# Optimization experiments

Hardware: AMD Instinct MI355X
Metric: run time of the kernel (lower is better)

The kernel has to match this reference:

```python
import jax, jax.numpy as jnp
from jax import lax
import numpy as np

NSTEP, NGRID, MU = 365, 4000, 8
STAIND = NSTEP - 1          # time index providing static parameters
TDLST = [1, 2, 3, 4, 5]     # 1-based indices of dynamic parameters
HBV_LO = jnp.array([0.0, 1.0, 0.005, 0.005, 0.0, 0.0, 0.005, 0.005, 0.0, 0.0, 0.0], jnp.float32)
HBV_HI = jnp.array([1.0, 2000.0, 0.995, 0.995, 1.0, 7.0, 0.995, 0.995, 1.0, 1.0, 1.0], jnp.float32)
SMIN = 1e-4                 # clamp floor for states
CAPMIN = 0.005 / 4          # floor for derived capacities

# ---- MARRMoT-style flux helpers (all elementwise) ----

def split_1(p1, In):
    return p1 * In

def soilmoisture_1(S1, S1max, S2, S2max):
    mask = (S1 / S1max < S2 / S2max).astype(S1.dtype)
    return (S2 * S1max - S1 * S2max) / (S1max + S2max) * mask

def soilmoisture_2(S1, S1max, S2, S2max, S3, S3max):
    # water rebalance to equal relative storage (3 stores); flux drawn from S2
    mask = (S1 / S1max < (S2 + S3) / (S2max + S3max)).astype(S1.dtype)
    return (S2 * S1max - S1 * S2max) / (S1max + S2max + S3max) * mask

def evap_7(S, Smax, Ep, dt):
    return jnp.minimum(S / Smax * Ep, S / dt)

def evap_1(S, Ep, dt):
    return jnp.minimum(Ep, S / dt)

def saturation_1(In, S, Smax):
    return In * (S >= Smax).astype(In.dtype)

def interflow_5(p1, S):
    return p1 * S

def baseflow_1(p1, S):
    return p1 * S

def percolation_4(pbase, zperc, rexp, deficit, defmax, S, Smax, dt):
    pc = pbase * (1.0 + zperc * (deficit / defmax) ** (1.0 + rexp)) * S / Smax
    return jnp.maximum(0.0, jnp.minimum(pc, S / dt))

def deficit_dist(S1, S1max, S2, S2max):
    d1 = jnp.maximum(0.0, 1.0 - S1 / S1max)
    d2 = jnp.maximum(0.0, 1.0 - S2 / S2max)
    tot = d1 + d2
    return jnp.where(tot > 0, d1 / jnp.where(tot > 0, tot, 1.0), S1max / (S1max + S2max))


def _forward(x, parameters):
    Nstep, Ngrid = x.shape[0], x.shape[1]
    mu = parameters.shape[3]
    P_ = x[:, :, 0]   # [Nstep, Ngrid]
    Ep_ = x[:, :, 2]  # [Nstep, Ngrid]

    # scale raw [0,1] params to physical ranges
    parT = HBV_LO[None, None, :, None] + parameters * (HBV_HI - HBV_LO)[None, None, :, None]
    parsta = parT[STAIND]  # [Ngrid, 11, mu] static params
    dyn = np.zeros(11, dtype=bool)
    for ix in TDLST:
        dyn[ix - 1] = True
    dyn = jnp.asarray(dyn)
    # dydrop=0 -> dynamic params always used on tdlst slots, static elsewhere
    parhbv = jnp.where(dyn[None, None, :, None], parT, parsta[None])  # [Nstep,Ngrid,11,mu]

    S0 = jnp.full((Ngrid, mu), 0.001, x.dtype)

    def step(carry, inp):
        S1, S2, S3, S4, S5 = carry
        Pt, Ept, par = inp            # par: [Ngrid, 11, mu]
        P = Pt[:, None]               # [Ngrid, 1] broadcasts against [Ngrid, mu]
        Ep = Ept[:, None]
        pctim, smax, f1, f2, kuz, rexp, f3, f4, pfree, klzp, klzs = [par[:, i, :] for i in range(11)]

        uztwm = f1 * smax
        uzfwm = jnp.maximum(CAPMIN, f2 * (smax - uztwm))
        lztwm = jnp.maximum(CAPMIN, f3 * (smax - uztwm - uzfwm))
        lzfwpm = jnp.maximum(CAPMIN, f4 * (smax - uztwm - uzfwm - lztwm))
        lzfwsm = jnp.maximum(CAPMIN, (1.0 - f4) * (smax - uztwm - uzfwm - lztwm))
        pbase = lzfwpm * klzp + lzfwsm * klzs
        denom = lzfwsm * klzs + lzfwpm * klzp
        zperc = jnp.minimum(1e5, (lztwm + lzfwsm * (1.0 - klzs)) / denom + lzfwpm * (1.0 - klzp) / denom)
        dt = 1.0

        flux_qdir = split_1(pctim, P)
        flux_peff = split_1(1.0 - pctim, P)
        flux_ru = soilmoisture_1(S1, uztwm, S2, uzfwm)
        flux_euztw = evap_7(S1, uztwm, Ep, dt)
        flux_twexu = saturation_1(flux_peff, S1, uztwm)
        flux_qsur = saturation_1(flux_twexu, S2, uzfwm)
        flux_qint = interflow_5(kuz, S2)
        flux_euzfw = evap_1(S2, jnp.maximum(0.0, Ep - flux_euztw), dt)
        deficit = (jnp.maximum(1e-8, lztwm - S3) + jnp.maximum(1e-8, lzfwpm - S4)
                   + jnp.maximum(1e-8, lzfwsm - S5))
        defmax = jnp.maximum(1e-8, lztwm + lzfwpm + lzfwsm)
        flux_pc = percolation_4(pbase, zperc, rexp, deficit, defmax, S2, uzfwm, dt)
        flux_pctw = split_1(1.0 - pfree, flux_pc)
        flux_elztw = evap_7(S3, lztwm, jnp.maximum(0.0, Ep - flux_euztw - flux_euzfw), dt)
        flux_twexl = saturation_1(flux_pctw, S3, lztwm)
        fp = deficit_dist(S4, lzfwpm, S5, lzfwsm)
        fs = deficit_dist(S5, lzfwsm, S4, lzfwpm)
        flux_twexlp = split_1(fp, flux_twexl)
        flux_twexls = split_1(fs, flux_twexl)
        flux_pcfwp = split_1(pfree * fp, flux_pc)
        flux_pcfws = split_1(pfree * fs, flux_pc)
        flux_rlp = soilmoisture_2(S3, lztwm, S4, lzfwpm, S5, lzfwsm)
        flux_rls = soilmoisture_2(S3, lztwm, S5, lzfwsm, S4, lzfwpm)
        flux_qbfp = baseflow_1(klzp, S4)
        flux_qbfs = baseflow_1(klzs, S5)

        nS1 = jnp.maximum(S1 + flux_peff + flux_ru - flux_euztw - flux_twexu, SMIN)
        nS2 = jnp.maximum(S2 + flux_twexu - flux_euzfw - flux_qsur - flux_qint - flux_ru - flux_pc, SMIN)
        nS3 = jnp.maximum(S3 + flux_pctw + flux_rlp + flux_rls - flux_elztw - flux_twexl, SMIN)
        nS4 = jnp.maximum(S4 + flux_twexlp + flux_pcfwp - flux_rlp - flux_qbfp, SMIN)
        nS5 = jnp.maximum(S5 + flux_twexls + flux_pcfws - flux_rls - flux_qbfs, SMIN)

        qsim = flux_qdir + flux_qsur + flux_qint + flux_qbfp + flux_qbfs
        et = flux_euztw + flux_euzfw + flux_elztw
        return (nS1, nS2, nS3, nS4, nS5), (qsim, et)

    _, (Qsimmu, ETmu) = lax.scan(step, (S0, S0, S0, S0, S0), (P_, Ep_, parhbv))
    Qs = Qsimmu.mean(-1, keepdims=True)      # muwts=None -> mean over components
    ETave = ETmu.mean(-1, keepdims=True)
    return jnp.concatenate([Qs, ETave], axis=-1)  # [Nstep, Ngrid, 2]


def setup_inputs() -> dict:
    key = jax.random.key(0)
    k1, k2 = jax.random.split(key)
    x = jax.random.uniform(k1, (NSTEP, NGRID, 3), dtype=jnp.float32)
    parameters = jax.random.uniform(k2, (NSTEP, NGRID, 11, MU), dtype=jnp.float32)
    return {"x": x, "parameters": parameters}


def reference(x, parameters):
    return _forward(x, parameters)
```

## Files before the change

kernel.cpp:

```cpp
#include <hip/hip_runtime.h>
#include <stdint.h>

#define NSTEP 365
#define NGRID 4000
#define CAPMIN 0.00125f
#define SMINV 0.0001f
#define PSTR_DW (NGRID * 88)
#define XSTR_DW (NGRID * 3)

#define RAW_SLOT 384
#define RAW_REG  (5 * RAW_SLOT)
#define DER_SLOT 960
#define DER_REG  (5 * DER_SLOT)
#define DER_BASE 5760
#define SMQ_BASE 15360
#define SME_BASE 15680

typedef __attribute__((address_space(3))) uint32_t lds_u32_t;
typedef __attribute__((address_space(1))) uint32_t glb_u32_t;

__device__ __forceinline__ void dma4(const float* g, float* l) {
    __builtin_amdgcn_global_load_lds((const glb_u32_t*)(const void*)g,
                                     (lds_u32_t*)(void*)l, 4, 0, 0);
}

__device__ __forceinline__ float frcp(float x) { return __builtin_amdgcn_rcpf(x); }
__device__ __forceinline__ float fexp2(float x) { return __builtin_amdgcn_exp2f(x); }
__device__ __forceinline__ float flog2(float x) { return __builtin_amdgcn_logf(x); }

__device__ __forceinline__ void issue_slot(const float* pp, const float* px,
                                           int t, float* dst) {
    const float* pj = pp + (size_t)t * PSTR_DW;
    dma4(pj,      dst);
    dma4(pj + 8,  dst + 64);
    dma4(pj + 16, dst + 128);
    dma4(pj + 24, dst + 192);
    dma4(pj + 32, dst + 256);
    dma4(px + (size_t)t * XSTR_DW, dst + 320);
}

__global__ __launch_bounds__(192, 1) void sacsma_kernel(
    const float* __restrict__ x,
    const float* __restrict__ par,
    float* __restrict__ out)
{
    __shared__ __align__(16) float lds[16000];

    const int wave = threadIdx.x >> 6;
    const int lane = threadIdx.x & 63;
    const int g0   = blockIdx.x * 8;
    const int gl   = lane >> 3;
    const int mu   = lane & 7;
    const int g    = g0 + gl;

    if (wave == 0) {
        const float* pp = par + (size_t)g * 88 + mu;
        int xl = lane; if (xl >= 24) xl -= 24; if (xl >= 24) xl -= 24;
        const int xq = xl / 3;
        const float* px = x + (g0 + xq) * 3 + (xl - xq * 3);

        #pragma unroll
        for (int j = 0; j < 5; ++j)
            issue_slot(pp, px, j, lds + j * RAW_SLOT);

        for (int i = 0; i < 75; ++i) {
            asm volatile("s_waitcnt vmcnt(0)" ::: "memory");
            if (i <= 71) {
                const int b = i + 1;
                float* dst = lds + (b % 3) * RAW_REG;
                const int tb = 5 * b;
                #pragma unroll
                for (int j = 0; j < 5; ++j)
                    issue_slot(pp, px, tb + j, dst + j * RAW_SLOT);
            }
            asm volatile("s_barrier" ::: "memory");
        }
    } else if (wave == 1) {
        const float* ps = par + ((size_t)(NSTEP - 1) * NGRID + g) * 88 + mu;
        const float f3   = 0.005f + ps[6 * 8] * 0.99f;
        const float f4   = 0.005f + ps[7 * 8] * 0.99f;
        const float klzp = ps[9 * 8];
        const float klzs = ps[10 * 8];

        for (int i = 0; i < 75; ++i) {
            if (i >= 1 && i <= 73) {
                const int b = i - 1;
                const float* rreg = lds + (b % 3) * RAW_REG;
                float* dreg = lds + DER_BASE + (b & 1) * DER_REG;
                #pragma unroll
                for (int j = 0; j < 5; ++j) {
                    const float* rb = rreg + j * RAW_SLOT;
                    float* db = dreg + j * DER_SLOT;

                    const float c0 = rb[lane];
                    const float c1 = rb[64 + lane];
                    const float c2 = rb[128 + lane];
                    const float c3 = rb[192 + lane];
                    const float c4 = rb[256 + lane];
                    const float P  = rb[320 + gl * 3];
                    const float Ep = rb[322 + gl * 3];

                    const float smaxv = 1.0f + c1 * 1999.0f;
                    const float f1 = 0.005f + c2 * 0.99f;
                    const float f2 = 0.005f + c3 * 0.99f;
                    const float uztwm = f1 * smaxv;
                    float rem = smaxv - uztwm;
                    const float uzfwm = fmaxf(CAPMIN, f2 * rem);
                    rem -= uzfwm;
                    const float lztwm = fmaxf(CAPMIN, f3 * rem);
                    rem -= lztwm;
                    const float lzfwpm = fmaxf(CAPMIN, f4 * rem);
                    const float lzfwsm = fmaxf(CAPMIN, (1.0f - f4) * rem);
                    const float pbase = lzfwpm * klzp + lzfwsm * klzs;
                    const float pz = fminf(lztwm + lzfwsm * (1.0f - klzs)
                                           + lzfwpm * (1.0f - klzp),
                                           100000.0f * pbase);
                    const float inv_uztwm = frcp(uztwm);
                    const float inv_uzfwm = frcp(uzfwm);
                    const float inv_lztwm = frcp(lztwm);
                    const float inv_uzsum = frcp(uztwm + uzfwm);
                    const float qdir = c0 * P;
                    const float peff = (1.0f - c0) * P;

                    float2* d2 = reinterpret_cast<float2*>(db);
                    d2[0 * 64 + lane] = make_float2(qdir, peff);
                    d2[1 * 64 + lane] = make_float2(Ep, c4);
                    d2[2 * 64 + lane] = make_float2(uztwm, uzfwm);
                    d2[3 * 64 + lane] = make_float2(inv_uztwm, inv_uzfwm);
                    d2[4 * 64 + lane] = make_float2(inv_uzsum, lztwm);
                    d2[5 * 64 + lane] = make_float2(inv_lztwm, pbase);
                    d2[6 * 64 + lane] = make_float2(lzfwpm, lzfwsm);
                    db[896 + lane] = pz;
                }
                asm volatile("s_waitcnt lgkmcnt(0)" ::: "memory");
            }
            asm volatile("s_barrier" ::: "memory");
        }
    } else {
        const float* ps = par + ((size_t)(NSTEP - 1) * NGRID + g) * 88 + mu;
        const float e1    = 1.0f + ps[5 * 8] * 7.0f;
        const float pfree = ps[8 * 8];
        const float klzp  = ps[9 * 8];
        const float klzs  = ps[10 * 8];

        float S1 = 0.001f, S2 = 0.001f, S3 = 0.001f, S4 = 0.001f, S5 = 0.001f;
        float* smq = lds + SMQ_BASE;
        float* sme = lds + SME_BASE;

        for (int i = 0; i < 75; ++i) {
            if (i >= 2) {
                const int b = i - 2;
                const float* dreg = lds + DER_BASE + (b & 1) * DER_REG;
                #pragma unroll
                for (int j = 0; j < 5; ++j) {
                    const float* db = dreg + j * DER_SLOT;
                    const float2* d2 = reinterpret_cast<const float2*>(db);
                    const float2 v0 = d2[0 * 64 + lane];
                    const float2 v1 = d2[1 * 64 + lane];
                    const float2 v2 = d2[2 * 64 + lane];
                    const float2 v3 = d2[3 * 64 + lane];
                    const float2 v4 = d2[4 * 64 + lane];
                    const float2 v5 = d2[5 * 64 + lane];
                    const float2 v6 = d2[6 * 64 + lane];
                    const float pz = db[896 + lane];
                    const float qdir = v0.x, peff = v0.y;
                    const float Ep = v1.x, kuz = v1.y;
                    const float uztwm = v2.x, uzfwm = v2.y;
                    const float inv_uztwm = v3.x, inv_uzfwm = v3.y;
                    const float inv_uzsum = v4.x, lztwm = v4.y;
                    const float inv_lztwm = v5.x, pbase = v5.y;
                    const float lzfwpm = v6.x, lzfwsm = v6.y;

                    const float rud = S2 * uztwm - S1 * uzfwm;
                    const float ru  = (rud > 0.0f) ? rud * inv_uzsum : 0.0f;
                    const float euztw = fminf(S1 * inv_uztwm * Ep, S1);
                    const float twexu = (S1 >= uztwm) ? peff : 0.0f;
                    const float qsur  = (S2 >= uzfwm) ? twexu : 0.0f;
                    const float qint  = kuz * S2;
                    const float euzfw = fminf(fmaxf(0.0f, Ep - euztw), S2);

                    const float deficit = fmaxf(1e-8f, lztwm - S3)
                                        + fmaxf(1e-8f, lzfwpm - S4)
                                        + fmaxf(1e-8f, lzfwsm - S5);
                    const float defmax = lztwm + lzfwpm + lzfwsm;
                    const float inv_defmax = frcp(defmax);
                    const float powterm = fexp2(e1 * flog2(deficit * inv_defmax));
                    float pc = (pbase + pz * powterm) * S2 * inv_uzfwm;
                    pc = fmaxf(0.0f, fminf(pc, S2));

                    const float pctw  = (1.0f - pfree) * pc;
                    const float elztw = fminf(S3 * inv_lztwm
                                              * fmaxf(0.0f, Ep - euztw - euzfw), S3);
                    const float twexl = (S3 >= lztwm) ? pctw : 0.0f;

                    const float aa  = fmaxf(0.0f, lzfwpm - S4) * lzfwsm;
                    const float bb  = fmaxf(0.0f, lzfwsm - S5) * lzfwpm;
                    const float den = aa + bb;
                    const float pm  = lzfwpm + lzfwsm;
                    const float fp  = ((den > 0.0f) ? aa : lzfwpm)
                                    * frcp((den > 0.0f) ? den : pm);
                    const float fs  = 1.0f - fp;

                    const float twexlp = fp * twexl;
                    const float twexls = fs * twexl;
                    const float pcfwp  = pfree * fp * pc;
                    const float pcfws  = pfree * fs * pc;

                    const bool rlm = S3 * pm < (S4 + S5) * lztwm;
                    const float rlp = rlm ? (S4 * lztwm - S3 * lzfwpm) * inv_defmax : 0.0f;
                    const float rls = rlm ? (S5 * lztwm - S3 * lzfwsm) * inv_defmax : 0.0f;

                    const float qbfp = klzp * S4;
                    const float qbfs = klzs * S5;

                    S1 = fmaxf(S1 + peff + ru - euztw - twexu, SMINV);
                    S2 = fmaxf(S2 + twexu - euzfw - qsur - qint - ru - pc, SMINV);
                    S3 = fmaxf(S3 + pctw + rlp + rls - elztw - twexl, SMINV);
                    S4 = fmaxf(S4 + twexlp + pcfwp - rlp - qbfp, SMINV);
                    S5 = fmaxf(S5 + twexls + pcfws - rls - qbfs, SMINV);

                    smq[j * 64 + lane] = qdir + qsur + qint + qbfp + qbfs;
                    sme[j * 64 + lane] = euztw + euzfw + elztw;
                }

                if (lane < 40) {
                    const int s  = lane >> 3;
                    const int gg = lane & 7;
                    const float4* q4 = reinterpret_cast<const float4*>(&smq[s * 64 + gg * 8]);
                    const float4* e4 = reinterpret_cast<const float4*>(&sme[s * 64 + gg * 8]);
                    const float4 qa = q4[0], qb = q4[1];
                    const float4 ea = e4[0], eb = e4[1];
                    const float qsum = ((qa.x + qa.y) + (qa.z + qa.w))
                                     + ((qb.x + qb.y) + (qb.z + qb.w));
                    const float esum = ((ea.x + ea.y) + (ea.z + ea.w))
                                     + ((eb.x + eb.y) + (eb.z + eb.w));
                    float2 o = make_float2(qsum * 0.125f, esum * 0.125f);
                    *reinterpret_cast<float2*>(
                        out + ((size_t)(5 * b + s) * NGRID + g0 + gg) * 2) = o;
                }
            }
            asm volatile("s_barrier" ::: "memory");
        }
    }
}

extern "C" void kernel_launch(void* const* d_in, const int* in_sizes, int n_in,
                              void* d_out, int out_size, void* d_ws, size_t ws_size,
                              hipStream_t stream) {
    const float* x   = (const float*)d_in[0];
    const float* par = (const float*)d_in[1];
    float* out = (float*)d_out;

    sacsma_kernel<<<NGRID / 8, 192, 0, stream>>>(x, par, out);
}
```

Measured before the change: 121.6 us.

## Deepen raw-load ring, shrink derived buffer, batch LDS reads before recurrence

The raw-input ring grows from three to four regions. The loader wave now waits with vmcnt(30) instead of vmcnt(0), so one batch of DMA stays in flight across the barrier. The derived buffer drops qdir/peff/Ep/kuz, which the recurrence wave now reads straight from the raw ring, and inv_defmax is precomputed in the producer instead. The recurrence wave issues all LDS reads for its five steps up front, taking LDS latency off the serial chain. The costs are higher register pressure and a more intricate buffer-lifetime scheme: the raw region must stay valid for two extra stages, and the 4-region layout has to fit under DER_BASE.

```diff
diff --git a/kernel.cpp b/kernel.cpp
--- a/kernel.cpp
+++ b/kernel.cpp
@@ -10,9 +10,9 @@
 
 #define RAW_SLOT 384
 #define RAW_REG  (5 * RAW_SLOT)
-#define DER_SLOT 960
+#define DER_BASE 7680
+#define DER_SLOT 768
 #define DER_REG  (5 * DER_SLOT)
-#define DER_BASE 5760
 #define SMQ_BASE 15360
 #define SME_BASE 15680
 
@@ -39,6 +39,70 @@
     dma4(px + (size_t)t * XSTR_DW, dst + 320);
 }
 
+#define RDS(j)                                                               \
+    const float  c0_##j = rreg[(j) * RAW_SLOT + lane];                       \
+    const float  kz_##j = rreg[(j) * RAW_SLOT + 256 + lane];                 \
+    const float  Pp_##j = rreg[(j) * RAW_SLOT + 320 + gl3];                  \
+    const float  Ee_##j = rreg[(j) * RAW_SLOT + 322 + gl3];                  \
+    const float2 dA_##j = dreg[(j) * 384 + lane];                            \
+    const float2 dB_##j = dreg[(j) * 384 + 64 + lane];                       \
+    const float2 dC_##j = dreg[(j) * 384 + 128 + lane];                      \
+    const float2 dD_##j = dreg[(j) * 384 + 192 + lane];                      \
+    const float2 dE_##j = dreg[(j) * 384 + 256 + lane];                      \
+    const float2 dF_##j = dreg[(j) * 384 + 320 + lane];
+
+#define STEP(j) do {                                                         \
+    const float uztwm = dA_##j.x, uzfwm = dA_##j.y;                          \
+    const float inv_uztwm = dB_##j.x, inv_uzfwm = dB_##j.y;                  \
+    const float inv_uzsum = dC_##j.x, lztwm = dC_##j.y;                      \
+    const float inv_lztwm = dD_##j.x, pbase = dD_##j.y;                      \
+    const float lzfwpm = dE_##j.x, lzfwsm = dE_##j.y;                        \
+    const float pz = dF_##j.x, inv_defmax = dF_##j.y;                        \
+    const float Ep = Ee_##j, kuz = kz_##j;                                   \
+    const float qdir = c0_##j * Pp_##j;                                      \
+    const float peff = Pp_##j - qdir;                                        \
+    const float rud  = S2 * uztwm - S1 * uzfwm;                              \
+    const float ru   = (rud > 0.0f) ? rud * inv_uzsum : 0.0f;                \
+    const float euztw = fminf(S1 * inv_uztwm * Ep, S1);                      \
+    const float twexu = (S1 >= uztwm) ? peff : 0.0f;                         \
+    const float qsur  = (S2 >= uzfwm) ? twexu : 0.0f;                        \
+    const float qint  = kuz * S2;                                            \
+    const float euzfw = fminf(fmaxf(0.0f, Ep - euztw), S2);                  \
+    const float deficit = fmaxf(1e-8f, lztwm - S3)                           \
+                        + fmaxf(1e-8f, lzfwpm - S4)                          \
+                        + fmaxf(1e-8f, lzfwsm - S5);                         \
+    const float powterm = fexp2(e1 * flog2(deficit * inv_defmax));           \
+    float pc = (pbase + pz * powterm) * (S2 * inv_uzfwm);                    \
+    pc = fmaxf(0.0f, fminf(pc, S2));                                         \
+    const float pctw  = (1.0f - pfree) * pc;                                 \
+    const float elztw = fminf(S3 * inv_lztwm                                 \
+                              * fmaxf(0.0f, Ep - euztw - euzfw), S3);        \
+    const float twexl = (S3 >= lztwm) ? pctw : 0.0f;                         \
+    const float aa  = fmaxf(0.0f, lzfwpm - S4) * lzfwsm;                     \
+    const float bb  = fmaxf(0.0f, lzfwsm - S5) * lzfwpm;                     \
+    const float den = aa + bb;                                               \
+    const float pm  = lzfwpm + lzfwsm;                                       \
+    const float fp  = ((den > 0.0f) ? aa : lzfwpm)                           \
+                    * frcp((den > 0.0f) ? den : pm);                         \
+    const float fs  = 1.0f - fp;                                             \
+    const float twexlp = fp * twexl;                                         \
+    const float twexls = fs * twexl;                                         \
+    const float pcfwp  = pfree * fp * pc;                                    \
+    const float pcfws  = pfree * fs * pc;                                    \
+    const bool rlm = S3 * pm < (S4 + S5) * lztwm;                            \
+    const float rlp = rlm ? (S4 * lztwm - S3 * lzfwpm) * inv_defmax : 0.0f;  \
+    const float rls = rlm ? (S5 * lztwm - S3 * lzfwsm) * inv_defmax : 0.0f;  \
+    const float qbfp = klzp * S4;                                            \
+    const float qbfs = klzs * S5;                                            \
+    S1 = fmaxf(S1 + peff + ru - euztw - twexu, SMINV);                       \
+    S2 = fmaxf(S2 + twexu - euzfw - qsur - qint - ru - pc, SMINV);           \
+    S3 = fmaxf(S3 + pctw + rlp + rls - elztw - twexl, SMINV);                \
+    S4 = fmaxf(S4 + twexlp + pcfwp - rlp - qbfp, SMINV);                     \
+    S5 = fmaxf(S5 + twexls + pcfws - rls - qbfs, SMINV);                     \
+    smq[(j) * 64 + lane] = qdir + qsur + qint + qbfp + qbfs;                 \
+    sme[(j) * 64 + lane] = euztw + euzfw + elztw;                            \
+} while (0)
+
 __global__ __launch_bounds__(192, 1) void sacsma_kernel(
     const float* __restrict__ x,
     const float* __restrict__ par,
@@ -64,14 +128,16 @@
             issue_slot(pp, px, j, lds + j * RAW_SLOT);
 
         for (int i = 0; i < 75; ++i) {
-            asm volatile("s_waitcnt vmcnt(0)" ::: "memory");
             if (i <= 71) {
                 const int b = i + 1;
-                float* dst = lds + (b % 3) * RAW_REG;
+                float* dst = lds + (b & 3) * RAW_REG;
                 const int tb = 5 * b;
                 #pragma unroll
                 for (int j = 0; j < 5; ++j)
                     issue_slot(pp, px, tb + j, dst + j * RAW_SLOT);
+                asm volatile("s_waitcnt vmcnt(30)" ::: "memory");
+            } else {
+                asm volatile("s_waitcnt vmcnt(0)" ::: "memory");
             }
             asm volatile("s_barrier" ::: "memory");
         }
@@ -85,20 +151,16 @@
         for (int i = 0; i < 75; ++i) {
             if (i >= 1 && i <= 73) {
                 const int b = i - 1;
-                const float* rreg = lds + (b % 3) * RAW_REG;
-                float* dreg = lds + DER_BASE + (b & 1) * DER_REG;
+                const float* rreg = lds + (b & 3) * RAW_REG;
+                float* dregf = lds + DER_BASE + (b & 1) * DER_REG;
                 #pragma unroll
                 for (int j = 0; j < 5; ++j) {
                     const float* rb = rreg + j * RAW_SLOT;
-                    float* db = dreg + j * DER_SLOT;
-
-                    const float c0 = rb[lane];
+                    float2* db = reinterpret_cast<float2*>(dregf + j * DER_SLOT);
+
                     const float c1 = rb[64 + lane];
                     const float c2 = rb[128 + lane];
                     const float c3 = rb[192 + lane];
-                    const float c4 = rb[256 + lane];
-                    const float P  = rb[320 + gl * 3];
-                    const float Ep = rb[322 + gl * 3];
 
                     const float smaxv = 1.0f + c1 * 1999.0f;
                     const float f1 = 0.005f + c2 * 0.99f;
@@ -119,18 +181,14 @@
                     const float inv_uzfwm = frcp(uzfwm);
                     const float inv_lztwm = frcp(lztwm);
                     const float inv_uzsum = frcp(uztwm + uzfwm);
-                    const float qdir = c0 * P;
-                    const float peff = (1.0f - c0) * P;
-
-                    float2* d2 = reinterpret_cast<float2*>(db);
-                    d2[0 * 64 + lane] = make_float2(qdir, peff);
-                    d2[1 * 64 + lane] = make_float2(Ep, c4);
-                    d2[2 * 64 + lane] = make_float2(uztwm, uzfwm);
-                    d2[3 * 64 + lane] = make_float2(inv_uztwm, inv_uzfwm);
-                    d2[4 * 64 + lane] = make_float2(inv_uzsum, lztwm);
-                    d2[5 * 64 + lane] = make_float2(inv_lztwm, pbase);
-                    d2[6 * 64 + lane] = make_float2(lzfwpm, lzfwsm);
-                    db[896 + lane] = pz;
+                    const float inv_defmax = frcp(lztwm + lzfwpm + lzfwsm);
+
+                    db[0 * 64 + lane] = make_float2(uztwm, uzfwm);
+                    db[1 * 64 + lane] = make_float2(inv_uztwm, inv_uzfwm);
+                    db[2 * 64 + lane] = make_float2(inv_uzsum, lztwm);
+                    db[3 * 64 + lane] = make_float2(inv_lztwm, pbase);
+                    db[4 * 64 + lane] = make_float2(lzfwpm, lzfwsm);
+                    db[5 * 64 + lane] = make_float2(pz, inv_defmax);
                 }
                 asm volatile("s_waitcnt lgkmcnt(0)" ::: "memory");
             }
@@ -146,82 +204,17 @@
         float S1 = 0.001f, S2 = 0.001f, S3 = 0.001f, S4 = 0.001f, S5 = 0.001f;
         float* smq = lds + SMQ_BASE;
         float* sme = lds + SME_BASE;
+        const int gl3 = gl * 3;
 
         for (int i = 0; i < 75; ++i) {
             if (i >= 2) {
                 const int b = i - 2;
-                const float* dreg = lds + DER_BASE + (b & 1) * DER_REG;
-                #pragma unroll
-                for (int j = 0; j < 5; ++j) {
-                    const float* db = dreg + j * DER_SLOT;
-                    const float2* d2 = reinterpret_cast<const float2*>(db);
-                    const float2 v0 = d2[0 * 64 + lane];
-                    const float2 v1 = d2[1 * 64 + lane];
-                    const float2 v2 = d2[2 * 64 + lane];
-                    const float2 v3 = d2[3 * 64 + lane];
-                    const float2 v4 = d2[4 * 64 + lane];
-                    const float2 v5 = d2[5 * 64 + lane];
-                    const float2 v6 = d2[6 * 64 + lane];
-                    const float pz = db[896 + lane];
-                    const float qdir = v0.x, peff = v0.y;
-                    const float Ep = v1.x, kuz = v1.y;
-                    const float uztwm = v2.x, uzfwm = v2.y;
-                    const float inv_uztwm = v3.x, inv_uzfwm = v3.y;
-                    const float inv_uzsum = v4.x, lztwm = v4.y;
-                    const float inv_lztwm = v5.x, pbase = v5.y;
-                    const float lzfwpm = v6.x, lzfwsm = v6.y;
-
-                    const float rud = S2 * uztwm - S1 * uzfwm;
-                    const float ru  = (rud > 0.0f) ? rud * inv_uzsum : 0.0f;
-                    const float euztw = fminf(S1 * inv_uztwm * Ep, S1);
-                    const float twexu = (S1 >= uztwm) ? peff : 0.0f;
-                    const float qsur  = (S2 >= uzfwm) ? twexu : 0.0f;
-                    const float qint  = kuz * S2;
-                    const float euzfw = fminf(fmaxf(0.0f, Ep - euztw), S2);
-
-                    const float deficit = fmaxf(1e-8f, lztwm - S3)
-                                        + fmaxf(1e-8f, lzfwpm - S4)
-                                        + fmaxf(1e-8f, lzfwsm - S5);
-                    const float defmax = lztwm + lzfwpm + lzfwsm;
-                    const float inv_defmax = frcp(defmax);
-                    const float powterm = fexp2(e1 * flog2(deficit * inv_defmax));
-                    float pc = (pbase + pz * powterm) * S2 * inv_uzfwm;
-                    pc = fmaxf(0.0f, fminf(pc, S2));
-
-                    const float pctw  = (1.0f - pfree) * pc;
-                    const float elztw = fminf(S3 * inv_lztwm
-                                              * fmaxf(0.0f, Ep - euztw - euzfw), S3);
-                    const float twexl = (S3 >= lztwm) ? pctw : 0.0f;
-
-                    const float aa  = fmaxf(0.0f, lzfwpm - S4) * lzfwsm;
-                    const float bb  = fmaxf(0.0f, lzfwsm - S5) * lzfwpm;
-                    const float den = aa + bb;
-                    const float pm  = lzfwpm + lzfwsm;
-                    const float fp  = ((den > 0.0f) ? aa : lzfwpm)
-                                    * frcp((den > 0.0f) ? den : pm);
-                    const float fs  = 1.0f - fp;
-
-                    const float twexlp = fp * twexl;
-                    const float twexls = fs * twexl;
-                    const float pcfwp  = pfree * fp * pc;
-                    const float pcfws  = pfree * fs * pc;
-
-                    const bool rlm = S3 * pm < (S4 + S5) * lztwm;
-                    const float rlp = rlm ? (S4 * lztwm - S3 * lzfwpm) * inv_defmax : 0.0f;
-                    const float rls = rlm ? (S5 * lztwm - S3 * lzfwsm) * inv_defmax : 0.0f;
-
-                    const float qbfp = klzp * S4;
-                    const float qbfs = klzs * S5;
-
-                    S1 = fmaxf(S1 + peff + ru - euztw - twexu, SMINV);
-                    S2 = fmaxf(S2 + twexu - euzfw - qsur - qint - ru - pc, SMINV);
-                    S3 = fmaxf(S3 + pctw + rlp + rls - elztw - twexl, SMINV);
-                    S4 = fmaxf(S4 + twexlp + pcfwp - rlp - qbfp, SMINV);
-                    S5 = fmaxf(S5 + twexls + pcfws - rls - qbfs, SMINV);
-
-                    smq[j * 64 + lane] = qdir + qsur + qint + qbfp + qbfs;
-                    sme[j * 64 + lane] = euztw + euzfw + elztw;
-                }
+                const float* rreg = lds + (b & 3) * RAW_REG;
+                const float2* dreg = reinterpret_cast<const float2*>(
+                    lds + DER_BASE + (b & 1) * DER_REG);
+
+                RDS(0) RDS(1) RDS(2) RDS(3) RDS(4)
+                STEP(0); STEP(1); STEP(2); STEP(3); STEP(4);
 
                 if (lane < 40) {
                     const int s  = lane >> 3;
```

Result: faster. 106.5 us (-12.5%).
